# Kernel optimization log

Hardware: AMD Instinct MI355X
Metric: run time of the kernel (lower is better)

The kernel has to match this reference:

```python
import jax, jax.numpy as jnp
import numpy as np

IN_C, OUT_C, K = 32, 3, 4
FT_DIM = IN_C // 2            # 16
LIN_IN = 4 + FT_DIM           # 20
D = IN_C * OUT_C * K * K      # 1536
D8, D4, D2 = D // 8, D // 4, D // 2


def _geometry(h_in, w_in, h_out, w_out, k):
    # numpy replica of get_offset_scale (all-static shapes)
    ih = np.arange(1, h_out + 1, dtype=np.float32)
    iw = np.arange(1, w_out + 1, dtype=np.float32)
    sh, sw = float(h_out) / h_in, float(w_out) / w_in
    ch = ih / sh + 0.5 * (1 - 1 / sh) - 1.0
    cw = iw / sw + 0.5 * (1 - 1 / sw) - 1.0
    s = -((k - 1) // 2)
    gh = np.floor(np.floor(ch)[:, None] + np.arange(s, k + s, dtype=np.float32)).reshape(-1)
    gw = np.floor(np.floor(cw)[:, None] + np.arange(s, k + s, dtype=np.float32)).reshape(-1)
    IH, IW = np.meshgrid(gh, gw, indexing='ij')                 # [h*k, w*k]
    indice = np.stack([IH, IW], -1).reshape(h_out, k, w_out, k, 2).transpose(0, 2, 1, 3, 4)  # [h,w,k,k,2]
    CH, CW = np.meshgrid(ch, cw, indexing='ij')
    center_hw = np.stack([CH, CW], -1).reshape(h_out, w_out, 1, 1, 2)
    c = -s
    offset = indice[:, :, c:c + 1, c:c + 1] - center_hw          # [h,w,1,1,2]
    off_scale = np.concatenate([
        offset,
        np.full((h_out, w_out, 1, 1, 1), sh, np.float32),
        np.full((h_out, w_out, 1, 1, 1), sw, np.float32)], -1).transpose(4, 0, 1, 2, 3)  # [4,h,w,1,1]
    ind = indice.astype(np.int64)
    center_ind = np.floor(center_hw).astype(np.int64)
    pad = int(max(-ind.min(), max((ind[..., 0] - h_in + 1).max(), (ind[..., 1] - w_in + 1).max())))
    return jnp.asarray(off_scale, jnp.float32), ind, center_ind, pad


def _pad_select(t, ind, pad):
    tp = jnp.pad(t, ((0, 0), (0, 0), (pad, pad), (pad, pad)), mode='reflect')
    return tp[:, :, ind[..., 0] + pad, ind[..., 1] + pad]   # [bs,C,*ind.shape[:-1]]


def setup_inputs() -> dict:
    key = jax.random.key(0)
    ks = jax.random.split(key, 16)
    p = lambda k, shp, sc: (jax.random.normal(k, shp, jnp.float32) * sc)
    inp = {
        'lr_features': jax.random.normal(ks[0], (2, IN_C, 48, 48), jnp.float32),
        'kernel_pc': jax.random.normal(ks[1], (2, 10, 48, 48), jnp.float32),
        'h_out': 192, 'w_out': 192,
        'ft_w': p(ks[2], (FT_DIM, IN_C, 4, 4), 0.05), 'ft_b': jnp.zeros((FT_DIM,), jnp.float32),
        'l1w1': p(ks[3], (LIN_IN, D8), 0.1), 'l1b1': jnp.zeros((D8,), jnp.float32),
        'l1w2': p(ks[4], (D8, D8), 0.05), 'l1b2': jnp.zeros((D8,), jnp.float32),
        'l2w1': p(ks[5], (LIN_IN, D8), 0.1), 'l2b1': jnp.zeros((D8,), jnp.float32),
        'l2w2': p(ks[6], (D8, D8), 0.05), 'l2b2': jnp.zeros((D8,), jnp.float32),
        'l3w1': p(ks[7], (D4, D2), 0.03), 'l3b1': jnp.zeros((D2,), jnp.float32),
        'l3w2': p(ks[8], (D2, D), 0.02), 'l3b2': jnp.zeros((D,), jnp.float32),
    }
    return inp


def reference(lr_features, kernel_pc, h_out, w_out, ft_w, ft_b,
              l1w1, l1b1, l1w2, l1b2, l2w1, l2b1, l2w2, l2b2,
              l3w1, l3b1, l3w2, l3b2):
    bs, cn, h_in, w_in = lr_features.shape
    off_scale, ind, center_ind, pad = _geometry(h_in, w_in, h_out, w_out, K)

    # gather kernel_size^2 neighbor pixels per output location
    sel = _pad_select(lr_features, ind, pad)                    # [bs,cn,h,w,K,K]
    sel = sel.transpose(0, 2, 3, 1, 4, 5).reshape(bs, h_out, w_out, cn * K * K)

    # feature_trans conv (reflect pad (1,2,1,2), 4x4, VALID)
    xp = jnp.pad(lr_features, ((0, 0), (0, 0), (1, 2), (1, 2)), mode='reflect')
    ft = jax.lax.conv_general_dilated(xp, ft_w, (1, 1), 'VALID',
                                      dimension_numbers=('NCHW', 'OIHW', 'NCHW'))
    ft = ft + ft_b[None, :, None, None]                         # [bs,FT_DIM,h_in,w_in]

    srf = _pad_select(ft, center_ind, pad)                      # [bs,FT_DIM,h,w,1,1]
    osb = jnp.broadcast_to(off_scale[None], (bs, 4, h_out, w_out, 1, 1))
    osf = jnp.concatenate([srf, osb], axis=1)[..., 0, 0].transpose(0, 2, 3, 1)  # [bs,h,w,LIN_IN]

    # offscale2weight: per-pixel MLP producing dynamic conv weights
    f1 = jnp.tanh(osf @ l1w1 + l1b1) @ l1w2 + l1b2
    f2 = jnp.tanh(osf @ l2w1 + l2b1) @ l2w2 + l2b2
    f = jnp.tanh(jnp.concatenate([f1 * f2, f1], axis=-1))
    f = f @ l3w1 + l3b1
    f = jnp.where(f > 0, f, 0.01 * f)                           # LeakyReLU
    w = (f @ l3w2 + l3b2).reshape(bs, h_out, w_out, OUT_C, cn * K * K)

    out = jnp.einsum('bhwk,bhwok->bhwo', sel, w)                # slice_mul
    return jnp.tanh(out.transpose(0, 3, 1, 2))                  # [bs,OUT_C,h_out,w_out]
```

## Files before the change

### kernel.cpp

```cpp
#include <hip/hip_runtime.h>
#include <math.h>

#define H_IN   48
#define W_IN   48
#define INC    32
#define OUTC   3
#define FT     16
#define Dn     1536
#define D8n    192
#define D4n    384
#define D2n    768

typedef _Float16 h16;
typedef _Float16 f16x8 __attribute__((ext_vector_type(8)));
typedef _Float16 f16x4 __attribute__((ext_vector_type(4)));
typedef float    f32x4 __attribute__((ext_vector_type(4)));

#define MFMA16(a, b, c) __builtin_amdgcn_mfma_f32_16x16x32_f16((a), (b), (c), 0, 0, 0)

__device__ __forceinline__ int reflect48(int i) {
    return (i < 0) ? -i : ((i > 47) ? 94 - i : i);
}

__device__ __forceinline__ float tanhf_fast(float x) {
    float e = __expf(2.f * x);
    return 1.f - 2.f / (e + 1.f);
}

#define SWZ(p, bc) ((bc) ^ (((p) & 7) << 4))

__global__ __launch_bounds__(256) void ft_kernel(const float* __restrict__ lr,
                                                 const float* __restrict__ ft_w,
                                                 const float* __restrict__ ft_b,
                                                 float* __restrict__ ftmap) {
    int idx = blockIdx.x * 256 + threadIdx.x;
    if (idx >= 2 * FT * H_IN * W_IN) return;
    int x = idx % W_IN;
    int y = (idx / W_IN) % H_IN;
    int o = (idx / (W_IN * H_IN)) % FT;
    int bb = idx / (W_IN * H_IN * FT);
    float acc = ft_b[o];
    for (int c = 0; c < INC; ++c) {
        const float* lrc = lr + ((bb * INC + c) * H_IN) * W_IN;
        const float* wc  = ft_w + ((o * INC + c) * 4) * 4;
        #pragma unroll
        for (int dy = 0; dy < 4; ++dy) {
            int ry = reflect48(y + dy - 1);
            #pragma unroll
            for (int dx = 0; dx < 4; ++dx) {
                int rx = reflect48(x + dx - 1);
                acc += lrc[ry * W_IN + rx] * wc[dy * 4 + dx];
            }
        }
    }
    ftmap[idx] = acc;
}

__global__ __launch_bounds__(256) void prep_kernel(const float* __restrict__ l1w2,
                                                   const float* __restrict__ l2w2,
                                                   const float* __restrict__ l3w1,
                                                   const float* __restrict__ l3w2,
                                                   h16* __restrict__ w12t, h16* __restrict__ w22t,
                                                   h16* __restrict__ w31t, h16* __restrict__ w32t) {
    __shared__ float tile[32][33];
    int bid = blockIdx.x;
    const float* src; h16* dst; int K, N, t0;
    if (bid < 36)      { src = l1w2; dst = w12t; K = 192; N = 192;  t0 = 0; }
    else if (bid < 72) { src = l2w2; dst = w22t; K = 192; N = 192;  t0 = 36; }
    else if (bid < 360){ src = l3w1; dst = w31t; K = 384; N = 768;  t0 = 72; }
    else               { src = l3w2; dst = w32t; K = 768; N = 1536; t0 = 360; }
    int t = bid - t0;
    int ntx = N >> 5;
    int kt = t / ntx, nt = t - kt * ntx;
    int k0 = kt << 5, n0 = nt << 5;
    int tx = threadIdx.x & 31, ty = threadIdx.x >> 5;
    #pragma unroll
    for (int i = 0; i < 4; ++i)
        tile[ty + i * 8][tx] = src[(k0 + ty + i * 8) * N + n0 + tx];
    __syncthreads();
    #pragma unroll
    for (int i = 0; i < 4; ++i)
        dst[(n0 + ty + i * 8) * K + k0 + tx] = (h16)tile[tx][ty + i * 8];
}

#define A_OFF_H1   0
#define A_OFF_H2   12288
#define A_OFF_OSF  24576
#define A_OFF_F    0
#define A_OFF_G    0
#define A_S_BYTES  49152

__global__ __launch_bounds__(256, 3) void fused_a(
    const float* __restrict__ ftmap,
    const float* __restrict__ l1w1, const float* __restrict__ l1b1,
    const float* __restrict__ l2w1, const float* __restrict__ l2b1,
    const float* __restrict__ l1b2, const float* __restrict__ l2b2,
    const float* __restrict__ l3b1,
    const h16* __restrict__ W12T, const h16* __restrict__ W22T,
    const h16* __restrict__ W31T,
    h16* __restrict__ Gf)
{
    __shared__ __align__(16) char S[A_S_BYTES];

    const int tid  = threadIdx.x;
    const int lane = tid & 63;
    const int wv   = tid >> 6;
    const int bid  = blockIdx.x;
    const int b    = bid / 1152;
    const int rem  = bid % 1152;
    const int h    = rem / 6;
    const int w0   = (rem % 6) * 32;

    const float ch = (h + 1) * 0.25f - 0.625f;
    const int   fh = (int)floorf(ch);
    const float offh = (float)fh - ch;
    const int   rfh = reflect48(fh);

    float* s_osf = (float*)(S + A_OFF_OSF);

    if (tid < 32) {
        int w = w0 + tid;
        float cw = (w + 1) * 0.25f - 0.625f;
        int fw = (int)floorf(cw);
        float* o = s_osf + tid * 20;
        o[16] = offh; o[17] = (float)fw - cw; o[18] = 4.f; o[19] = 4.f;
    }
    {
        int p = tid >> 3;
        int c0 = (tid & 7) * 2;
        int w = w0 + p;
        float cw = (w + 1) * 0.25f - 0.625f;
        int rfw = reflect48((int)floorf(cw));
        float* o = s_osf + p * 20;
        o[c0]     = ftmap[((b * FT + c0) * H_IN + rfh) * W_IN + rfw];
        o[c0 + 1] = ftmap[((b * FT + c0 + 1) * H_IN + rfh) * W_IN + rfw];
    }
    __syncthreads();

    for (int idx = tid; idx < 2 * 32 * D8n; idx += 256) {
        int br = idx / 6144;
        int r2 = idx - br * 6144;
        int p  = r2 / D8n;
        int j  = r2 - p * D8n;
        const float* W = br ? l2w1 : l1w1;
        const float* B = br ? l2b1 : l1b1;
        const float* o = s_osf + p * 20;
        float acc = B[j];
        #pragma unroll
        for (int i = 0; i < 20; ++i) acc += o[i] * W[i * D8n + j];
        int base = br ? A_OFF_H2 : A_OFF_H1;
        *(h16*)(S + base + p * 384 + SWZ(p, j * 2)) = (h16)tanhf_fast(acc);
    }
    __syncthreads();

    f16x8 Ah[2][2][6];
    {
        int pr = lane & 15, kg = (lane >> 4) << 3;
        #pragma unroll
        for (int br = 0; br < 2; ++br)
            #pragma unroll
            for (int rt = 0; rt < 2; ++rt) {
                int p = rt * 16 + pr;
                #pragma unroll
                for (int kf = 0; kf < 6; ++kf) {
                    int k0 = kf * 32 + kg;
                    Ah[br][rt][kf] = *(const f16x8*)(S + (br ? A_OFF_H2 : A_OFF_H1) + p * 384 + SWZ(p, k0 * 2));
                }
            }
    }
    __syncthreads();

    {
        int pr = lane & 15, kg = (lane >> 4) << 3;
        #pragma unroll
        for (int cc = 0; cc < 3; ++cc) {
            int c = wv * 3 + cc;
            int n = c * 16 + pr;
            f32x4 a00 = {0.f,0.f,0.f,0.f}, a01 = a00, a10 = a00, a11 = a00;
            #pragma unroll
            for (int kf = 0; kf < 6; ++kf) {
                int koff = kf * 32 + kg;
                f16x8 b0 = *(const f16x8*)(W12T + n * D8n + koff);
                f16x8 b1 = *(const f16x8*)(W22T + n * D8n + koff);
                a00 = MFMA16(Ah[0][0][kf], b0, a00);
                a01 = MFMA16(Ah[0][1][kf], b0, a01);
                a10 = MFMA16(Ah[1][0][kf], b1, a10);
                a11 = MFMA16(Ah[1][1][kf], b1, a11);
            }
            float bf1 = l1b2[n], bf2 = l2b2[n];
            #pragma unroll
            for (int rt = 0; rt < 2; ++rt) {
                #pragma unroll
                for (int r = 0; r < 4; ++r) {
                    int p = rt * 16 + ((lane >> 4) << 2) + r;
                    float f1 = (rt ? a01[r] : a00[r]) + bf1;
                    float f2 = (rt ? a11[r] : a10[r]) + bf2;
                    *(h16*)(S + A_OFF_F + p * 768 + SWZ(p, n * 2))         = (h16)tanhf_fast(f1 * f2);
                    *(h16*)(S + A_OFF_F + p * 768 + SWZ(p, (n + D8n) * 2)) = (h16)tanhf_fast(f1);
                }
            }
        }
    }
    __syncthreads();

    f16x8 Af[2][12];
    {
        int pr = lane & 15, kg = (lane >> 4) << 3;
        #pragma unroll
        for (int rt = 0; rt < 2; ++rt) {
            int p = rt * 16 + pr;
            #pragma unroll
            for (int kf = 0; kf < 12; ++kf) {
                int k0 = kf * 32 + kg;
                Af[rt][kf] = *(const f16x8*)(S + A_OFF_F + p * 768 + SWZ(p, k0 * 2));
            }
        }
    }
    __syncthreads();

    {
        int pr = lane & 15, kg = (lane >> 4) << 3;
        #pragma unroll
        for (int q = 0; q < 3; ++q) {
            int ntb = wv * 12 + q * 4;
            f32x4 acc[4][2];
            #pragma unroll
            for (int nn = 0; nn < 4; ++nn) { acc[nn][0] = (f32x4){0.f,0.f,0.f,0.f}; acc[nn][1] = acc[nn][0]; }
            for (int kf = 0; kf < 12; ++kf) {
                int koff = kf * 32 + kg;
                f16x8 bq[4];
                #pragma unroll
                for (int nn = 0; nn < 4; ++nn)
                    bq[nn] = *(const f16x8*)(W31T + ((ntb + nn) * 16 + pr) * D4n + koff);
                #pragma unroll
                for (int nn = 0; nn < 4; ++nn) {
                    acc[nn][0] = MFMA16(Af[0][kf], bq[nn], acc[nn][0]);
                    acc[nn][1] = MFMA16(Af[1][kf], bq[nn], acc[nn][1]);
                }
            }
            #pragma unroll
            for (int nn = 0; nn < 4; ++nn) {
                int n = (ntb + nn) * 16 + pr;
                float bb = l3b1[n];
                #pragma unroll
                for (int rt = 0; rt < 2; ++rt) {
                    #pragma unroll
                    for (int r = 0; r < 4; ++r) {
                        int p = rt * 16 + ((lane >> 4) << 2) + r;
                        float gv = acc[nn][rt][r] + bb;
                        gv = (gv > 0.f) ? gv : 0.01f * gv;
                        *(h16*)(S + A_OFF_G + p * 1536 + SWZ(p, n * 2)) = (h16)gv;
                    }
                }
            }
        }
    }
    __syncthreads();

    {
        int pr = lane & 15, kg = lane >> 4;
        int ptg0 = (b * 192 + h) * 12 + (w0 >> 4);
        #pragma unroll
        for (int i = 0; i < 12; ++i) {
            int pair = wv * 12 + i;
            int rt = pair / 24, kf = pair % 24;
            int p = rt * 16 + pr;
            f16x8 v = *(const f16x8*)(S + A_OFF_G + p * 1536 + SWZ(p, (kf * 32 + kg * 8) * 2));
            size_t e = ((size_t)((ptg0 + rt) * 24 + kf) * 4 + kg) * 16 + pr;
            *(f16x8*)(Gf + e * 8) = v;
        }
    }
}

#define B_S_BYTES (65536 + 6144)

__global__ __launch_bounds__(512, 4) void gemm_b(
    const float* __restrict__ lr,
    const h16* __restrict__ Gf,
    const h16* __restrict__ W32T,
    const float* __restrict__ l3b2,
    float* __restrict__ out)
{
    __shared__ __align__(16) char S[B_S_BYTES];
    float* s_red = (float*)(S + 65536);

    const int tid  = threadIdx.x;
    const int lane = tid & 63;
    const int wvv  = tid >> 6;
    const int pr   = lane & 15;
    const int kg   = lane >> 4;

    const int bid = blockIdx.x;
    const int b   = bid / 576;
    const int rem = bid % 576;
    const int h   = rem / 3;
    const int w0  = (rem % 3) * 64;

    const float chh = (h + 1) * 0.25f - 0.625f;
    const int fh = (int)floorf(chh);

    {
        int k = tid;
        int c = k >> 4, k1 = (k >> 2) & 3, k2 = k & 3;
        int rh = reflect48(fh - 1 + k1);
        const float* lrrow = lr + ((b * INC + c) * H_IN + rh) * W_IN;
        #pragma unroll 8
        for (int p = 0; p < 64; ++p) {
            float cw = (w0 + p + 1) * 0.25f - 0.625f;
            int fw = (int)floorf(cw);
            float v = lrrow[reflect48(fw - 1 + k2)];
            *(h16*)(S + p * 1024 + ((k * 2) ^ ((p & 7) << 4))) = (h16)v;
        }
    }
    __syncthreads();

    {
        int p = tid >> 3, part = tid & 7;
        const char* selrow = (const char*)S + p * 1024;
        float s0 = 0.f, s1 = 0.f, s2 = 0.f;
        #pragma unroll
        for (int j = 0; j < 16; ++j) {
            int k = part * 64 + j * 4;
            f16x4 sl = *(const f16x4*)(selrow + ((k * 2) ^ ((p & 7) << 4)));
            float4 ba = *(const float4*)(l3b2 + k);
            float4 bbv = *(const float4*)(l3b2 + 512 + k);
            float4 bc = *(const float4*)(l3b2 + 1024 + k);
            #pragma unroll
            for (int r = 0; r < 4; ++r) {
                float sv = (float)sl[r];
                s0 += ((const float*)&ba)[r]  * sv;
                s1 += ((const float*)&bbv)[r] * sv;
                s2 += ((const float*)&bc)[r]  * sv;
            }
        }
        float* rr = s_red + ((size_t)part * 64 + p) * 3;
        rr[0] = s0; rr[1] = s1; rr[2] = s2;
    }
    __syncthreads();

    const int ptB = (b * 192 + h) * 12 + (w0 >> 4);

    f16x8 gB[4][3];
    {
        const h16* Gbase = Gf + (size_t)(kg * 16 + pr) * 8;
        #pragma unroll
        for (int pt = 0; pt < 4; ++pt)
            #pragma unroll
            for (int kfl = 0; kfl < 3; ++kfl)
                gB[pt][kfl] = *(const f16x8*)(Gbase +
                    ((size_t)((ptB + pt) * 24 + (wvv * 3 + kfl)) * 64) * 8);
    }

    const h16* Wbase = W32T + (size_t)pr * D2n + wvv * 96 + kg * 8;

    float acc0[4], acc1[4], acc2[4];
    #pragma unroll
    for (int pt = 0; pt < 4; ++pt) { acc0[pt] = 0.f; acc1[pt] = 0.f; acc2[pt] = 0.f; }

    const f32x4 z4 = {0.f, 0.f, 0.f, 0.f};

    f16x8 WaA0, WaA1, WaA2, WaB0, WaB1, WaB2;
    WaA0 = *(const f16x8*)(Wbase);
    WaA1 = *(const f16x8*)(Wbase + 32);
    WaA2 = *(const f16x8*)(Wbase + 64);

    #define STEP(NT, W0_, W1_, W2_, N0_, N1_, N2_, ACC) {                          \
        int ntn_ = (NT) + 1; ntn_ = (ntn_ > 95) ? 95 : ntn_;                       \
        const h16* wp_ = Wbase + (size_t)ntn_ * (16 * D2n);                        \
        N0_ = *(const f16x8*)(wp_);                                                \
        N1_ = *(const f16x8*)(wp_ + 32);                                           \
        N2_ = *(const f16x8*)(wp_ + 64);                                           \
        f32x4 w0_ = MFMA16(W0_, gB[0][0], z4);                                     \
        f32x4 w1_ = MFMA16(W0_, gB[1][0], z4);                                     \
        f32x4 w2_ = MFMA16(W0_, gB[2][0], z4);                                     \
        f32x4 w3_ = MFMA16(W0_, gB[3][0], z4);                                     \
        w0_ = MFMA16(W1_, gB[0][1], w0_);                                          \
        w1_ = MFMA16(W1_, gB[1][1], w1_);                                          \
        w2_ = MFMA16(W1_, gB[2][1], w2_);                                          \
        w3_ = MFMA16(W1_, gB[3][1], w3_);                                          \
        w0_ = MFMA16(W2_, gB[0][2], w0_);                                          \
        w1_ = MFMA16(W2_, gB[1][2], w1_);                                          \
        w2_ = MFMA16(W2_, gB[2][2], w2_);                                          \
        w3_ = MFMA16(W2_, gB[3][2], w3_);                                          \
        const int kbase_ = ((NT) & 31) * 16 + kg * 4;                              \
        {                                                                          \
            const int p_ = pr;                                                     \
            f16x4 sl_ = *(const f16x4*)(S + p_ * 1024 + ((kbase_ * 2) ^ ((p_ & 7) << 4))); \
            ACC[0] += w0_[0]*(float)sl_[0] + w0_[1]*(float)sl_[1]                  \
                    + w0_[2]*(float)sl_[2] + w0_[3]*(float)sl_[3];                 \
        }                                                                          \
        {                                                                          \
            const int p_ = 16 + pr;                                                \
            f16x4 sl_ = *(const f16x4*)(S + p_ * 1024 + ((kbase_ * 2) ^ ((p_ & 7) << 4))); \
            ACC[1] += w1_[0]*(float)sl_[0] + w1_[1]*(float)sl_[1]                  \
                    + w1_[2]*(float)sl_[2] + w1_[3]*(float)sl_[3];                 \
        }                                                                          \
        {                                                                          \
            const int p_ = 32 + pr;                                                \
            f16x4 sl_ = *(const f16x4*)(S + p_ * 1024 + ((kbase_ * 2) ^ ((p_ & 7) << 4))); \
            ACC[2] += w2_[0]*(float)sl_[0] + w2_[1]*(float)sl_[1]                  \
                    + w2_[2]*(float)sl_[2] + w2_[3]*(float)sl_[3];                 \
        }                                                                          \
        {                                                                          \
            const int p_ = 48 + pr;                                                \
            f16x4 sl_ = *(const f16x4*)(S + p_ * 1024 + ((kbase_ * 2) ^ ((p_ & 7) << 4))); \
            ACC[3] += w3_[0]*(float)sl_[0] + w3_[1]*(float)sl_[1]                  \
                    + w3_[2]*(float)sl_[2] + w3_[3]*(float)sl_[3];                 \
        }                                                                          \
    }

    for (int t = 0; t < 16; ++t) {
        STEP(2*t,     WaA0, WaA1, WaA2, WaB0, WaB1, WaB2, acc0)
        STEP(2*t + 1, WaB0, WaB1, WaB2, WaA0, WaA1, WaA2, acc0)
    }
    for (int t = 16; t < 32; ++t) {
        STEP(2*t,     WaA0, WaA1, WaA2, WaB0, WaB1, WaB2, acc1)
        STEP(2*t + 1, WaB0, WaB1, WaB2, WaA0, WaA1, WaA2, acc1)
    }
    for (int t = 32; t < 48; ++t) {
        STEP(2*t,     WaA0, WaA1, WaA2, WaB0, WaB1, WaB2, acc2)
        STEP(2*t + 1, WaB0, WaB1, WaB2, WaA0, WaA1, WaA2, acc2)
    }
    #undef STEP

    #pragma unroll
    for (int pt = 0; pt < 4; ++pt) {
        float v0 = acc0[pt], v1 = acc1[pt], v2 = acc2[pt];
        v0 += __shfl_xor(v0, 16); v0 += __shfl_xor(v0, 32);
        v1 += __shfl_xor(v1, 16); v1 += __shfl_xor(v1, 32);
        v2 += __shfl_xor(v2, 16); v2 += __shfl_xor(v2, 32);
        if (lane < 16) {
            float* r = s_red + ((size_t)wvv * 64 + pt * 16 + pr) * 3;
            r[0] += v0; r[1] += v1; r[2] += v2;
        }
    }
    __syncthreads();
    if (tid < 192) {
        int p = tid / 3, oc = tid % 3;
        float s = 0.f;
        #pragma unroll
        for (int wv2 = 0; wv2 < 8; ++wv2) s += s_red[((size_t)wv2 * 64 + p) * 3 + oc];
        out[((b * OUTC + oc) * 192 + h) * 192 + (w0 + p)] = tanhf_fast(s);
    }
}

__global__ __launch_bounds__(256, 2) void fused_fallback(
    const float* __restrict__ lr, const float* __restrict__ ftmap,
    const float* __restrict__ l1w1, const float* __restrict__ l1b1,
    const float* __restrict__ l2w1, const float* __restrict__ l2b1,
    const float* __restrict__ l1b2, const float* __restrict__ l2b2,
    const float* __restrict__ l3b1, const float* __restrict__ l3b2,
    const h16* __restrict__ W12T, const h16* __restrict__ W22T,
    const h16* __restrict__ W31T, const h16* __restrict__ W32T,
    float* __restrict__ out)
{
    __shared__ __align__(16) char S[63104];
    const int tid  = threadIdx.x;
    const int lane = tid & 63;
    const int wv   = tid >> 6;
    const int bid  = blockIdx.x;
    const int b    = bid / 1152;
    const int rem  = bid % 1152;
    const int h    = rem / 6;
    const int w0   = (rem % 6) * 32;

    const float ch = (h + 1) * 0.25f - 0.625f;
    const int   fh = (int)floorf(ch);
    const float offh = (float)fh - ch;
    const int   rfh = reflect48(fh);

    float* s_osf = (float*)(S + 24576);
    unsigned char* s_sc = (unsigned char*)(S + 61440);
    h16*   s_lrr = (h16*)(S + 49152);
    float* s_red = (float*)(S + 61568);

    if (tid < 128) {
        int p = tid >> 2, k2 = tid & 3;
        int w = w0 + p;
        float cw = (w + 1) * 0.25f - 0.625f;
        int fw = (int)floorf(cw);
        s_sc[p * 4 + k2] = (unsigned char)reflect48(fw - 1 + k2);
        if (k2 == 0) {
            float* o = s_osf + p * 20;
            o[16] = offh; o[17] = (float)fw - cw; o[18] = 4.f; o[19] = 4.f;
        }
    }
    {
        int p = tid >> 3;
        int c0 = (tid & 7) * 2;
        int w = w0 + p;
        float cw = (w + 1) * 0.25f - 0.625f;
        int rfw = reflect48((int)floorf(cw));
        float* o = s_osf + p * 20;
        o[c0]     = ftmap[((b * FT + c0) * H_IN + rfh) * W_IN + rfw];
        o[c0 + 1] = ftmap[((b * FT + c0 + 1) * H_IN + rfh) * W_IN + rfw];
    }
    for (int idx = tid; idx < 32 * 4 * 48; idx += 256) {
        int c = idx / 192, r2 = idx - c * 192, k1 = r2 / 48, col = r2 - k1 * 48;
        int row = reflect48(fh - 1 + k1);
        s_lrr[idx] = (h16)lr[((b * INC + c) * H_IN + row) * W_IN + col];
    }
    for (int idx = tid; idx < 4 * 32 * 3; idx += 256) s_red[idx] = 0.f;
    __syncthreads();

    for (int idx = tid; idx < 2 * 32 * D8n; idx += 256) {
        int br = idx / 6144;
        int r2 = idx - br * 6144;
        int p  = r2 / D8n;
        int j  = r2 - p * D8n;
        const float* W = br ? l2w1 : l1w1;
        const float* B = br ? l2b1 : l1b1;
        const float* o = s_osf + p * 20;
        float acc = B[j];
        #pragma unroll
        for (int i = 0; i < 20; ++i) acc += o[i] * W[i * D8n + j];
        int base = br ? 12288 : 0;
        *(h16*)(S + base + p * 384 + SWZ(p, j * 2)) = (h16)tanhf_fast(acc);
    }
    __syncthreads();

    f16x8 Ah[2][2][6];
    {
        int pr = lane & 15, kg = (lane >> 4) << 3;
        #pragma unroll
        for (int br = 0; br < 2; ++br)
            #pragma unroll
            for (int rt = 0; rt < 2; ++rt) {
                int p = rt * 16 + pr;
                #pragma unroll
                for (int kf = 0; kf < 6; ++kf)
                    Ah[br][rt][kf] = *(const f16x8*)(S + (br ? 12288 : 0) + p * 384 + SWZ(p, (kf * 32 + kg) * 2));
            }
    }
    __syncthreads();

    {
        int pr = lane & 15, kg = (lane >> 4) << 3;
        #pragma unroll
        for (int cc = 0; cc < 3; ++cc) {
            int c = wv * 3 + cc;
            int n = c * 16 + pr;
            f32x4 a00 = {0.f,0.f,0.f,0.f}, a01 = a00, a10 = a00, a11 = a00;
            #pragma unroll
            for (int kf = 0; kf < 6; ++kf) {
                int koff = kf * 32 + kg;
                f16x8 b0 = *(const f16x8*)(W12T + n * D8n + koff);
                f16x8 b1 = *(const f16x8*)(W22T + n * D8n + koff);
                a00 = MFMA16(Ah[0][0][kf], b0, a00);
                a01 = MFMA16(Ah[0][1][kf], b0, a01);
                a10 = MFMA16(Ah[1][0][kf], b1, a10);
                a11 = MFMA16(Ah[1][1][kf], b1, a11);
            }
            float bf1 = l1b2[n], bf2 = l2b2[n];
            #pragma unroll
            for (int rt = 0; rt < 2; ++rt)
                #pragma unroll
                for (int r = 0; r < 4; ++r) {
                    int p = rt * 16 + ((lane >> 4) << 2) + r;
                    float f1 = (rt ? a01[r] : a00[r]) + bf1;
                    float f2 = (rt ? a11[r] : a10[r]) + bf2;
                    *(h16*)(S + p * 768 + SWZ(p, n * 2))         = (h16)tanhf_fast(f1 * f2);
                    *(h16*)(S + p * 768 + SWZ(p, (n + D8n) * 2)) = (h16)tanhf_fast(f1);
                }
        }
    }
    __syncthreads();

    f16x8 Af[2][12];
    {
        int pr = lane & 15, kg = (lane >> 4) << 3;
        #pragma unroll
        for (int rt = 0; rt < 2; ++rt) {
            int p = rt * 16 + pr;
            #pragma unroll
            for (int kf = 0; kf < 12; ++kf)
                Af[rt][kf] = *(const f16x8*)(S + p * 768 + SWZ(p, (kf * 32 + kg) * 2));
        }
    }
    __syncthreads();

    {
        int pr = lane & 15, kg = (lane >> 4) << 3;
        #pragma unroll
        for (int q = 0; q < 3; ++q) {
            int ntb = wv * 12 + q * 4;
            f32x4 acc[4][2];
            #pragma unroll
            for (int nn = 0; nn < 4; ++nn) { acc[nn][0] = (f32x4){0.f,0.f,0.f,0.f}; acc[nn][1] = acc[nn][0]; }
            for (int kf = 0; kf < 12; ++kf) {
                int koff = kf * 32 + kg;
                f16x8 bq[4];
                #pragma unroll
                for (int nn = 0; nn < 4; ++nn)
                    bq[nn] = *(const f16x8*)(W31T + ((ntb + nn) * 16 + pr) * D4n + koff);
                #pragma unroll
                for (int nn = 0; nn < 4; ++nn) {
                    acc[nn][0] = MFMA16(Af[0][kf], bq[nn], acc[nn][0]);
                    acc[nn][1] = MFMA16(Af[1][kf], bq[nn], acc[nn][1]);
                }
            }
            #pragma unroll
            for (int nn = 0; nn < 4; ++nn) {
                int n = (ntb + nn) * 16 + pr;
                float bb = l3b1[n];
                #pragma unroll
                for (int rt = 0; rt < 2; ++rt)
                    #pragma unroll
                    for (int r = 0; r < 4; ++r) {
                        int p = rt * 16 + ((lane >> 4) << 2) + r;
                        float gv = acc[nn][rt][r] + bb;
                        gv = (gv > 0.f) ? gv : 0.01f * gv;
                        *(h16*)(S + p * 1536 + SWZ(p, n * 2)) = (h16)gv;
                    }
            }
        }
    }
    __syncthreads();

    {
        int pr = lane & 15, kg = (lane >> 4) << 3;
        float acc8[2][4];
        #pragma unroll
        for (int rt = 0; rt < 2; ++rt)
            #pragma unroll
            for (int r = 0; r < 4; ++r) acc8[rt][r] = 0.f;
        int cur_oc = (wv * 24) >> 5;

        for (int q = 0; q < 6; ++q) {
            int ntb = wv * 24 + q * 4;
            int oc = ntb >> 5;
            if (oc != cur_oc) {
                #pragma unroll
                for (int rt = 0; rt < 2; ++rt)
                    #pragma unroll
                    for (int r = 0; r < 4; ++r) {
                        float v = acc8[rt][r];
                        v += __shfl_xor(v, 1); v += __shfl_xor(v, 2);
                        v += __shfl_xor(v, 4); v += __shfl_xor(v, 8);
                        if ((lane & 15) == 0) {
                            int p = rt * 16 + ((lane >> 4) << 2) + r;
                            s_red[(wv * 32 + p) * 3 + cur_oc] += v;
                        }
                        acc8[rt][r] = 0.f;
                    }
                cur_oc = oc;
            }
            f32x4 acc[4][2];
            #pragma unroll
            for (int nn = 0; nn < 4; ++nn) { acc[nn][0] = (f32x4){0.f,0.f,0.f,0.f}; acc[nn][1] = acc[nn][0]; }
            for (int kf = 0; kf < 24; ++kf) {
                int koff = kf * 32 + kg;
                f16x8 a0 = *(const f16x8*)(S + pr * 1536 + SWZ(pr, koff * 2));
                int p1 = 16 + pr;
                f16x8 a1 = *(const f16x8*)(S + p1 * 1536 + SWZ(p1, koff * 2));
                f16x8 bq[4];
                #pragma unroll
                for (int nn = 0; nn < 4; ++nn)
                    bq[nn] = *(const f16x8*)(W32T + ((ntb + nn) * 16 + pr) * D2n + koff);
                #pragma unroll
                for (int nn = 0; nn < 4; ++nn) {
                    acc[nn][0] = MFMA16(a0, bq[nn], acc[nn][0]);
                    acc[nn][1] = MFMA16(a1, bq[nn], acc[nn][1]);
                }
            }
            #pragma unroll
            for (int nn = 0; nn < 4; ++nn) {
                int n = (ntb + nn) * 16 + pr;
                float wb = l3b2[n];
                int k  = n & 511;
                int c  = k >> 4, k1 = (k >> 2) & 3, k2 = k & 3;
                const h16* lrr = s_lrr + (c * 4 + k1) * 48;
                #pragma unroll
                for (int rt = 0; rt < 2; ++rt)
                    #pragma unroll
                    for (int r = 0; r < 4; ++r) {
                        int p = rt * 16 + ((lane >> 4) << 2) + r;
                        float sv = (float)lrr[s_sc[p * 4 + k2]];
                        acc8[rt][r] += (acc[nn][rt][r] + wb) * sv;
                    }
            }
        }
        #pragma unroll
        for (int rt = 0; rt < 2; ++rt)
            #pragma unroll
            for (int r = 0; r < 4; ++r) {
                float v = acc8[rt][r];
                v += __shfl_xor(v, 1); v += __shfl_xor(v, 2);
                v += __shfl_xor(v, 4); v += __shfl_xor(v, 8);
                if ((lane & 15) == 0) {
                    int p = rt * 16 + ((lane >> 4) << 2) + r;
                    s_red[(wv * 32 + p) * 3 + cur_oc] += v;
                }
            }
    }
    __syncthreads();

    if (tid < 96) {
        int p = tid / 3, oc = tid % 3;
        float s = s_red[(0 * 32 + p) * 3 + oc] + s_red[(1 * 32 + p) * 3 + oc]
                + s_red[(2 * 32 + p) * 3 + oc] + s_red[(3 * 32 + p) * 3 + oc];
        out[((b * OUTC + oc) * 192 + h) * 192 + (w0 + p)] = tanhf_fast(s);
    }
}

extern "C" void kernel_launch(void* const* d_in, const int* in_sizes, int n_in,
                              void* d_out, int out_size, void* d_ws, size_t ws_size,
                              hipStream_t stream) {
    const float* lr   = (const float*)d_in[0];
    const float* ft_w = (const float*)d_in[4];
    const float* ft_b = (const float*)d_in[5];
    const float* l1w1 = (const float*)d_in[6];
    const float* l1b1 = (const float*)d_in[7];
    const float* l1w2 = (const float*)d_in[8];
    const float* l1b2 = (const float*)d_in[9];
    const float* l2w1 = (const float*)d_in[10];
    const float* l2b1 = (const float*)d_in[11];
    const float* l2w2 = (const float*)d_in[12];
    const float* l2b2 = (const float*)d_in[13];
    const float* l3w1 = (const float*)d_in[14];
    const float* l3b1 = (const float*)d_in[15];
    const float* l3w2 = (const float*)d_in[16];
    const float* l3b2 = (const float*)d_in[17];
    float* outp = (float*)d_out;

    char* ws = (char*)d_ws;
    float* ftmap = (float*)(ws + 0);
    h16* w12t = (h16*)(ws + 294912);
    h16* w22t = (h16*)(ws + 368640);
    h16* w31t = (h16*)(ws + 442368);
    h16* w32t = (h16*)(ws + 1032192);
    h16* Gf   = (h16*)(ws + 3391488);

    hipLaunchKernelGGL(prep_kernel, dim3(1512), dim3(256), 0, stream,
                       l1w2, l2w2, l3w1, l3w2, w12t, w22t, w31t, w32t);
    hipLaunchKernelGGL(ft_kernel, dim3(288), dim3(256), 0, stream, lr, ft_w, ft_b, ftmap);

    if (ws_size >= (size_t)116637696) {
        hipLaunchKernelGGL(fused_a, dim3(2304), dim3(256), 0, stream,
                           ftmap, l1w1, l1b1, l2w1, l2b1,
                           l1b2, l2b2, l3b1,
                           w12t, w22t, w31t, Gf);
        hipLaunchKernelGGL(gemm_b, dim3(1152), dim3(512), 0, stream,
                           lr, Gf, w32t, l3b2, outp);
    } else {
        hipLaunchKernelGGL(fused_fallback, dim3(2304), dim3(256), 0, stream,
                           lr, ftmap,
                           l1w1, l1b1, l2w1, l2b1,
                           l1b2, l2b2, l3b1, l3b2,
                           w12t, w22t, w31t, w32t,
                           outp);
    }
}
```

Baseline: 698.7 us.

## Replace per-pixel unfolded selection tile with compact LR window in gemm_b

gemm_b used to build a 64x512 fp16 unfolded neighbourhood tile in shared memory (64KB). It now stages a small 32x4x20 fp32 window of the low-res input and indexes it per pixel with precomputed column offsets, both in the bias pass and in the MFMA epilogue. Shared memory drops from about 70KB to about 16KB, and launch bounds are raised to allow more resident blocks per CU. In exchange, the epilogue does scalar fp32 LDS reads with data-dependent offsets instead of vectorized f16x4 loads, which may cause bank conflicts. Raising the occupancy target may also cap registers and cause spills.

```diff
diff --git a/kernel.cpp b/kernel.cpp
--- a/kernel.cpp
+++ b/kernel.cpp
@@ -272,17 +272,15 @@
     }
 }
 
-#define B_S_BYTES (65536 + 6144)
-
-__global__ __launch_bounds__(512, 4) void gemm_b(
+__global__ __launch_bounds__(512, 8) void gemm_b(
     const float* __restrict__ lr,
     const h16* __restrict__ Gf,
     const h16* __restrict__ W32T,
     const float* __restrict__ l3b2,
     float* __restrict__ out)
 {
-    __shared__ __align__(16) char S[B_S_BYTES];
-    float* s_red = (float*)(S + 65536);
+    __shared__ float s_lr[32][4][20];
+    __shared__ float s_red[8][64][3];
 
     const int tid  = threadIdx.x;
     const int lane = tid & 63;
@@ -295,50 +293,53 @@
     const int rem = bid % 576;
     const int h   = rem / 3;
     const int w0  = (rem % 3) * 64;
+    const int w4  = w0 >> 2;
 
     const float chh = (h + 1) * 0.25f - 0.625f;
     const int fh = (int)floorf(chh);
 
-    {
-        int k = tid;
-        int c = k >> 4, k1 = (k >> 2) & 3, k2 = k & 3;
-        int rh = reflect48(fh - 1 + k1);
-        const float* lrrow = lr + ((b * INC + c) * H_IN + rh) * W_IN;
-        #pragma unroll 8
-        for (int p = 0; p < 64; ++p) {
-            float cw = (w0 + p + 1) * 0.25f - 0.625f;
-            int fw = (int)floorf(cw);
-            float v = lrrow[reflect48(fw - 1 + k2)];
-            *(h16*)(S + p * 1024 + ((k * 2) ^ ((p & 7) << 4))) = (h16)v;
-        }
+    for (int idx = tid; idx < 32 * 4 * 20; idx += 512) {
+        int c  = idx / 80;
+        int r2 = idx - c * 80;
+        int k1 = r2 / 20;
+        int j  = r2 - k1 * 20;
+        int row = reflect48(fh - 1 + k1);
+        int col = reflect48(w4 - 2 + j);
+        s_lr[c][k1][j] = lr[((b * INC + c) * H_IN + row) * W_IN + col];
     }
     __syncthreads();
 
     {
         int p = tid >> 3, part = tid & 7;
-        const char* selrow = (const char*)S + p * 1024;
+        int jbp = (int)floorf((w0 + p + 1) * 0.25f - 0.625f) - w4 + 1;
         float s0 = 0.f, s1 = 0.f, s2 = 0.f;
         #pragma unroll
         for (int j = 0; j < 16; ++j) {
-            int k = part * 64 + j * 4;
-            f16x4 sl = *(const f16x4*)(selrow + ((k * 2) ^ ((p & 7) << 4)));
-            float4 ba = *(const float4*)(l3b2 + k);
+            int k  = part * 4 + j * 32;
+            int c  = k >> 4;
+            int k1 = (k >> 2) & 3;
+            const float* lrow = &s_lr[c][k1][jbp];
+            float4 ba  = *(const float4*)(l3b2 + k);
             float4 bbv = *(const float4*)(l3b2 + 512 + k);
-            float4 bc = *(const float4*)(l3b2 + 1024 + k);
+            float4 bc  = *(const float4*)(l3b2 + 1024 + k);
             #pragma unroll
             for (int r = 0; r < 4; ++r) {
-                float sv = (float)sl[r];
+                float sv = lrow[r];
                 s0 += ((const float*)&ba)[r]  * sv;
                 s1 += ((const float*)&bbv)[r] * sv;
                 s2 += ((const float*)&bc)[r]  * sv;
             }
         }
-        float* rr = s_red + ((size_t)part * 64 + p) * 3;
-        rr[0] = s0; rr[1] = s1; rr[2] = s2;
+        s_red[part][p][0] = s0; s_red[part][p][1] = s1; s_red[part][p][2] = s2;
     }
     __syncthreads();
 
     const int ptB = (b * 192 + h) * 12 + (w0 >> 4);
+
+    const int jb0 = (int)floorf((w0 + pr      + 1) * 0.25f - 0.625f) - w4 + 1;
+    const int jb1 = (int)floorf((w0 + pr + 16 + 1) * 0.25f - 0.625f) - w4 + 1;
+    const int jb2 = (int)floorf((w0 + pr + 32 + 1) * 0.25f - 0.625f) - w4 + 1;
+    const int jb3 = (int)floorf((w0 + pr + 48 + 1) * 0.25f - 0.625f) - w4 + 1;
 
     f16x8 gB[4][3];
     {
@@ -382,31 +383,15 @@
         w1_ = MFMA16(W2_, gB[1][2], w1_);                                          \
         w2_ = MFMA16(W2_, gB[2][2], w2_);                                          \
         w3_ = MFMA16(W2_, gB[3][2], w3_);                                          \
-        const int kbase_ = ((NT) & 31) * 16 + kg * 4;                              \
-        {                                                                          \
-            const int p_ = pr;                                                     \
-            f16x4 sl_ = *(const f16x4*)(S + p_ * 1024 + ((kbase_ * 2) ^ ((p_ & 7) << 4))); \
-            ACC[0] += w0_[0]*(float)sl_[0] + w0_[1]*(float)sl_[1]                  \
-                    + w0_[2]*(float)sl_[2] + w0_[3]*(float)sl_[3];                 \
-        }                                                                          \
-        {                                                                          \
-            const int p_ = 16 + pr;                                                \
-            f16x4 sl_ = *(const f16x4*)(S + p_ * 1024 + ((kbase_ * 2) ^ ((p_ & 7) << 4))); \
-            ACC[1] += w1_[0]*(float)sl_[0] + w1_[1]*(float)sl_[1]                  \
-                    + w1_[2]*(float)sl_[2] + w1_[3]*(float)sl_[3];                 \
-        }                                                                          \
-        {                                                                          \
-            const int p_ = 32 + pr;                                                \
-            f16x4 sl_ = *(const f16x4*)(S + p_ * 1024 + ((kbase_ * 2) ^ ((p_ & 7) << 4))); \
-            ACC[2] += w2_[0]*(float)sl_[0] + w2_[1]*(float)sl_[1]                  \
-                    + w2_[2]*(float)sl_[2] + w2_[3]*(float)sl_[3];                 \
-        }                                                                          \
-        {                                                                          \
-            const int p_ = 48 + pr;                                                \
-            f16x4 sl_ = *(const f16x4*)(S + p_ * 1024 + ((kbase_ * 2) ^ ((p_ & 7) << 4))); \
-            ACC[3] += w3_[0]*(float)sl_[0] + w3_[1]*(float)sl_[1]                  \
-                    + w3_[2]*(float)sl_[2] + w3_[3]*(float)sl_[3];                 \
-        }                                                                          \
+        const float* lrow_ = &s_lr[(NT) & 31][kg][0];                              \
+        ACC[0] += w0_[0] * lrow_[jb0]     + w0_[1] * lrow_[jb0 + 1]                \
+                + w0_[2] * lrow_[jb0 + 2] + w0_[3] * lrow_[jb0 + 3];               \
+        ACC[1] += w1_[0] * lrow_[jb1]     + w1_[1] * lrow_[jb1 + 1]                \
+                + w1_[2] * lrow_[jb1 + 2] + w1_[3] * lrow_[jb1 + 3];               \
+        ACC[2] += w2_[0] * lrow_[jb2]     + w2_[1] * lrow_[jb2 + 1]                \
+                + w2_[2] * lrow_[jb2 + 2] + w2_[3] * lrow_[jb2 + 3];               \
+        ACC[3] += w3_[0] * lrow_[jb3]     + w3_[1] * lrow_[jb3 + 1]                \
+                + w3_[2] * lrow_[jb3 + 2] + w3_[3] * lrow_[jb3 + 3];               \
     }
 
     for (int t = 0; t < 16; ++t) {
@@ -430,7 +415,7 @@
         v1 += __shfl_xor(v1, 16); v1 += __shfl_xor(v1, 32);
         v2 += __shfl_xor(v2, 16); v2 += __shfl_xor(v2, 32);
         if (lane < 16) {
-            float* r = s_red + ((size_t)wvv * 64 + pt * 16 + pr) * 3;
+            float* r = &s_red[wvv][pt * 16 + pr][0];
             r[0] += v0; r[1] += v1; r[2] += v2;
         }
     }
@@ -439,7 +424,7 @@
         int p = tid / 3, oc = tid % 3;
         float s = 0.f;
         #pragma unroll
-        for (int wv2 = 0; wv2 < 8; ++wv2) s += s_red[((size_t)wv2 * 64 + p) * 3 + oc];
+        for (int wv2 = 0; wv2 < 8; ++wv2) s += s_red[wv2][p][oc];
         out[((b * OUTC + oc) * 192 + h) * 192 + (w0 + p)] = tanhf_fast(s);
     }
 }
```

Result: slower. 1.739 ms (+148.9%).
